# Performance work log

Hardware: AMD Instinct MI355X
Metric: run time of the kernel (lower is better)

The kernel has to match this reference:

```python
import jax, jax.numpy as jnp
import numpy as np

MAX_LENGTH = 10
SOS = 0
B, S, H, V = 256, 10, 1024, 32000


def setup_inputs() -> dict:
    key = jax.random.key(0)
    ks = jax.random.split(key, 16)
    p = lambda k, shp: (jax.random.normal(k, shp, dtype=jnp.float32) * 0.02)
    return {
        "encoder_outputs": jax.random.normal(ks[0], (B, S, H), dtype=jnp.float32),
        "encoder_hidden": jax.random.normal(ks[1], (1, B, H), dtype=jnp.float32),
        "target_tensor": jax.random.randint(ks[2], (B, MAX_LENGTH), 0, V),
        "emb": p(ks[3], (V, H)),
        "Wa": p(ks[4], (H, H)), "ba": p(ks[5], (H,)),
        "Ua": p(ks[6], (H, H)), "bua": p(ks[7], (H,)),
        "Va": p(ks[8], (1, H)), "bva": p(ks[9], (1,)),
        "W_ih": p(ks[10], (3 * H, 2 * H)), "W_hh": p(ks[11], (3 * H, H)),
        "b_ih": p(ks[12], (3 * H,)), "b_hh": p(ks[13], (3 * H,)),
        "W_out": p(ks[14], (V, H)), "b_out": p(ks[15], (V,)),
    }


def reference(encoder_outputs, encoder_hidden, target_tensor, emb, Wa, ba, Ua, bua,
              Va, bva, W_ih, W_hh, b_ih, b_hh, W_out, b_out):
    # Teacher forcing: input tokens are [SOS, tgt_0, ..., tgt_{T-2}]
    tokens = jnp.concatenate(
        [jnp.zeros((B, 1), dtype=target_tensor.dtype) + SOS,
         target_tensor[:, : MAX_LENGTH - 1]], axis=1)  # [B,T]
    keys = encoder_outputs                              # [B,S,H]
    keysW = jnp.einsum('bsh,oh->bso', keys, Wa) + ba    # Wa(keys), hoisted (step-invariant)

    def step(h, tok):                                   # h: [B,H], tok: [B]
        e = emb[tok]                                    # [B,H] (dropout in eval mode = identity)
        q = h @ Ua.T + bua                              # Ua(query): [B,H]
        score = jnp.tanh(keysW + q[:, None, :]) @ Va[0] + bva[0]  # [B,S]
        w = jax.nn.softmax(score, axis=1)               # softmax over seq dim
        ctx = jnp.einsum('bs,bsh->bh', w, keys)         # [B,H]
        x = jnp.concatenate([e, ctx], axis=1)           # [B,2H]
        gi = x @ W_ih.T + b_ih                          # [B,3H]
        gh = h @ W_hh.T + b_hh                          # [B,3H]
        r = jax.nn.sigmoid(gi[:, :H] + gh[:, :H])
        z = jax.nn.sigmoid(gi[:, H:2 * H] + gh[:, H:2 * H])
        n = jnp.tanh(gi[:, 2 * H:] + r * gh[:, 2 * H:])
        h_new = (1.0 - z) * n + z * h
        logits = h_new @ W_out.T + b_out                # [B,V]
        return h_new, (logits, w)

    h0 = encoder_hidden[0]                              # [B,H]
    h_last, (logits, attns) = jax.lax.scan(step, h0, tokens.T)  # logits:[T,B,V], attns:[T,B,S]
    dec_out = jax.nn.log_softmax(jnp.transpose(logits, (1, 0, 2)), axis=-1)  # [B,T,V]
    attentions = jnp.transpose(attns, (1, 0, 2)).reshape(B, MAX_LENGTH * S, 1)  # cat over dim=1
    return dec_out, h_last[None], attentions
```

## Files before the change

kernel.cpp:

```cpp
#include <hip/hip_runtime.h>
#include <hip/hip_bf16.h>
#include <math.h>

#define B_ 256
#define S_ 10
#define H_ 1024
#define V_ 32000
#define T_ 10

typedef __bf16 bf16x8 __attribute__((ext_vector_type(8)));
typedef float f32x4 __attribute__((ext_vector_type(4)));
typedef unsigned short u16;

__device__ inline u16 f2bu(float x) {
    __hip_bfloat16 b = __float2bfloat16(x);
    return *reinterpret_cast<unsigned short*>(&b);
}
__device__ inline float bu2f(u16 x) {
    unsigned u = (unsigned)x << 16;
    return __uint_as_float(u);
}

template<int BM, int BN, int BK, bool SCATTER, bool LSE, bool OUT16>
__global__ __launch_bounds__(256)
void gemm_bt(const u16* __restrict__ A, const u16* __restrict__ B,
             float* __restrict__ C, const float* __restrict__ bias,
             float* __restrict__ lse,
             int M, int N, int K, int ldc, int sb, int st)
{
    constexpr int WM = BM / 2, WN = BN / 2;
    constexpr int AT = WM / 16, BTT = WN / 16;
    constexpr int KS = BK / 32;

    constexpr int STG  = (BM + BN) * BK;
    constexpr int EPI  = 4 * 16 * (WN + 4) * 4;
    constexpr int SMEM = (2 * STG * 2) > EPI ? (2 * STG * 2) : EPI;
    __shared__ __align__(16) char smem[SMEM];
    u16* buf0 = (u16*)smem;
    u16* buf1 = buf0 + STG;

    const int tid  = threadIdx.x;
    const int wave = tid >> 6;
    const int lane = tid & 63;
    const int wm   = (wave >> 1) * WM;
    const int wn   = (wave & 1) * WN;

    int id  = blockIdx.y * gridDim.x + blockIdx.x;
    int nwg = gridDim.x * gridDim.y;
    int swz = id;
    if ((nwg & 7) == 0) swz = (id & 7) * (nwg >> 3) + (id >> 3);
    const int bm = (swz % gridDim.x) * BM;
    const int bn = (swz / gridDim.x) * BN;

    const int l16 = lane & 15;
    const int lk8 = (lane >> 4) * 8;

    f32x4 acc[AT][BTT];
#pragma unroll
    for (int i = 0; i < AT; ++i)
#pragma unroll
        for (int j = 0; j < BTT; ++j) {
            f32x4 z = {0.f, 0.f, 0.f, 0.f};
            acc[i][j] = z;
        }

    constexpr int ROUNDS_A = (BM * BK) / 2048;
    constexpr int ROUNDS_B = (BN * BK) / 2048;

    auto stage = [&](u16* dstA, int k0) {
        u16* dstB = dstA + BM * BK;
#pragma unroll
        for (int r = 0; r < ROUNDS_A; ++r) {
            int e   = r * 2048 + tid * 8;
            int row = e / BK;
            int kk  = e % BK;
            const u16* gp = A + (size_t)(bm + row) * K + k0 + kk;
            u16* lp = dstA + r * 2048 + wave * 512;
            __builtin_amdgcn_global_load_lds(
                (const __attribute__((address_space(1))) void*)gp,
                (__attribute__((address_space(3))) void*)lp, 16, 0, 0);
        }
        if constexpr (ROUNDS_B == 0) {
            if (tid < (BN * BK) / 8) {
                int e   = tid * 8;
                int row = e / BK;
                int kk  = e % BK;
                const u16* gp = B + (size_t)(bn + row) * K + k0 + kk;
                u16* lp = dstB + wave * 512;
                __builtin_amdgcn_global_load_lds(
                    (const __attribute__((address_space(1))) void*)gp,
                    (__attribute__((address_space(3))) void*)lp, 16, 0, 0);
            }
        } else {
#pragma unroll
            for (int r = 0; r < ROUNDS_B; ++r) {
                int e   = r * 2048 + tid * 8;
                int row = e / BK;
                int kk  = e % BK;
                const u16* gp = B + (size_t)(bn + row) * K + k0 + kk;
                u16* lp = dstB + r * 2048 + wave * 512;
                __builtin_amdgcn_global_load_lds(
                    (const __attribute__((address_space(1))) void*)gp,
                    (__attribute__((address_space(3))) void*)lp, 16, 0, 0);
            }
        }
    };

    const int nt = K / BK;
    stage(buf0, 0);
    asm volatile("s_waitcnt vmcnt(0)\n\ts_barrier" ::: "memory");

    int cur = 0;
    for (int t = 0; t < nt; ++t) {
        u16* As = cur ? buf1 : buf0;
        u16* Bs = As + BM * BK;
        u16* nxt = cur ? buf0 : buf1;
        if (t + 1 < nt) stage(nxt, (t + 1) * BK);

        bf16x8 af[KS][AT], bf[KS][BTT];
#pragma unroll
        for (int ks = 0; ks < KS; ++ks) {
#pragma unroll
            for (int i = 0; i < AT; ++i)
                af[ks][i] = *(const bf16x8*)(As + (wm + i * 16 + l16) * BK + ks * 32 + lk8);
#pragma unroll
            for (int j = 0; j < BTT; ++j)
                bf[ks][j] = *(const bf16x8*)(Bs + (wn + j * 16 + l16) * BK + ks * 32 + lk8);
        }
#pragma unroll
        for (int ks = 0; ks < KS; ++ks)
#pragma unroll
            for (int i = 0; i < AT; ++i)
#pragma unroll
                for (int j = 0; j < BTT; ++j)
                    acc[i][j] = __builtin_amdgcn_mfma_f32_16x16x32_bf16(
                        af[ks][i], bf[ks][j], acc[i][j], 0, 0, 0);

        if (t + 1 < nt) {
            asm volatile("s_waitcnt vmcnt(0)\n\ts_barrier" ::: "memory");
            cur ^= 1;
        }
    }
    __syncthreads();

    float (*eps)[16][WN + 4] = reinterpret_cast<float (*)[16][WN + 4]>(smem);
    constexpr int C4  = WN / 4;
    constexpr int RPI = 64 / C4;
    constexpr int STEPS = 16 / RPI;
    const int chunk = lane & (C4 - 1);
    const int rg    = lane / C4;
    const int col   = bn + wn + chunk * 4;
    const int lr4   = (lane >> 4) * 4;

    f32x4 bias4 = {0.f, 0.f, 0.f, 0.f};
    if (bias) bias4 = *(const f32x4*)(bias + col);

#pragma unroll
    for (int i = 0; i < AT; ++i) {
#pragma unroll
        for (int j = 0; j < BTT; ++j)
#pragma unroll
            for (int r = 0; r < 4; ++r)
                eps[wave][lr4 + r][j * 16 + l16] = acc[i][j][r];
#pragma unroll
        for (int s = 0; s < STEPS; ++s) {
            int rowL = s * RPI + rg;
            f32x4 v = *(const f32x4*)&eps[wave][rowL][chunk * 4];
            v += bias4;
            int row = bm + wm + i * 16 + rowL;
            size_t off;
            if constexpr (SCATTER)
                off = (size_t)(row & 255) * sb + (size_t)(row >> 8) * st + col;
            else
                off = (size_t)row * ldc + col;
            if constexpr (OUT16) {
                ushort4 o = {f2bu(v[0]), f2bu(v[1]), f2bu(v[2]), f2bu(v[3])};
                *(ushort4*)((u16*)C + off) = o;
            } else if constexpr (SCATTER) {
                __builtin_nontemporal_store(v, (f32x4*)(C + off));
            } else {
                *(f32x4*)(C + off) = v;
            }
            if constexpr (LSE) {
                float es = expf(v[0]) + expf(v[1]) + expf(v[2]) + expf(v[3]);
#pragma unroll
                for (int o = C4 / 2; o > 0; o >>= 1)
                    es += __shfl_xor(es, o, 64);
                if (chunk == 0) atomicAdd(&lse[row], es);
            }
        }
    }
}

__global__ __launch_bounds__(256)
void attn_gru(const float* __restrict__ keysW, const float* __restrict__ qgh,
              const float* __restrict__ Va, const float* __restrict__ bva,
              const float* __restrict__ gie_t, const u16* __restrict__ KW2,
              float* __restrict__ h, u16* __restrict__ Hall_t,
              float* __restrict__ hlast, float* __restrict__ attn_out, int t)
{
    const int b = blockIdx.x;
    const int tid = threadIdx.x;
    const int lane = tid & 63, wave = tid >> 6;
    const float* qb = qgh + (size_t)b * 4096;
    const float* kW = keysW + (size_t)b * S_ * H_;

    float vh[4], qh[4];
#pragma unroll
    for (int j = 0; j < 4; ++j) {
        int hh = tid + j * 256;
        vh[j] = Va[hh]; qh[j] = qb[hh];
    }

    __shared__ float lred[4][S_];
    __shared__ float wsm[S_];

#pragma unroll
    for (int s = 0; s < S_; ++s) {
        float p = 0.f;
#pragma unroll
        for (int j = 0; j < 4; ++j)
            p += vh[j] * tanhf(kW[s * H_ + tid + j * 256] + qh[j]);
        for (int off = 32; off > 0; off >>= 1) p += __shfl_down(p, off, 64);
        if (lane == 0) lred[wave][s] = p;
    }
    __syncthreads();
    if (tid == 0) {
        float sc[S_], mx = -1e30f;
        for (int s = 0; s < S_; ++s) {
            sc[s] = lred[0][s] + lred[1][s] + lred[2][s] + lred[3][s] + bva[0];
            mx = fmaxf(mx, sc[s]);
        }
        float sum = 0.f;
        for (int s = 0; s < S_; ++s) { sc[s] = expf(sc[s] - mx); sum += sc[s]; }
        float inv = 1.f / sum;
        for (int s = 0; s < S_; ++s) wsm[s] = sc[s] * inv;
    }
    __syncthreads();
    if (tid < S_) attn_out[(size_t)b * 100 + t * 10 + tid] = wsm[tid];

    const int i4 = tid * 4;
    float ar[4] = {0,0,0,0}, az[4] = {0,0,0,0}, an[4] = {0,0,0,0};
    const u16* kwb = KW2 + (size_t)b * (S_ * 3072);
#pragma unroll
    for (int s = 0; s < S_; ++s) {
        float w = wsm[s];
        const u16* kws = kwb + s * 3072;
        ushort4 vr = *(const ushort4*)(kws + i4);
        ushort4 vz = *(const ushort4*)(kws + 1024 + i4);
        ushort4 vn = *(const ushort4*)(kws + 2048 + i4);
        ar[0] += w * bu2f(vr.x); ar[1] += w * bu2f(vr.y);
        ar[2] += w * bu2f(vr.z); ar[3] += w * bu2f(vr.w);
        az[0] += w * bu2f(vz.x); az[1] += w * bu2f(vz.y);
        az[2] += w * bu2f(vz.z); az[3] += w * bu2f(vz.w);
        an[0] += w * bu2f(vn.x); an[1] += w * bu2f(vn.y);
        an[2] += w * bu2f(vn.z); an[3] += w * bu2f(vn.w);
    }

    const float* ghp = qgh + (size_t)b * 4096 + 1024;
    const float* gip = gie_t + (size_t)b * 3072;
    float4 g_r = *(const float4*)(gip + i4);
    float4 g_z = *(const float4*)(gip + 1024 + i4);
    float4 g_n = *(const float4*)(gip + 2048 + i4);
    float4 h_r = *(const float4*)(ghp + i4);
    float4 h_z = *(const float4*)(ghp + 1024 + i4);
    float4 h_n = *(const float4*)(ghp + 2048 + i4);
    float4 hold = *(const float4*)(h + (size_t)b * 1024 + i4);

    float hv[4];
#pragma unroll
    for (int r = 0; r < 4; ++r) {
        float gr = (&g_r.x)[r] + ar[r];
        float gz = (&g_z.x)[r] + az[r];
        float gn = (&g_n.x)[r] + an[r];
        float rr = 1.f / (1.f + expf(-(gr + (&h_r.x)[r])));
        float zz = 1.f / (1.f + expf(-(gz + (&h_z.x)[r])));
        float nn = tanhf(gn + rr * (&h_n.x)[r]);
        hv[r] = (1.f - zz) * nn + zz * (&hold.x)[r];
    }
    float4 hv4 = {hv[0], hv[1], hv[2], hv[3]};
    *(float4*)(h + (size_t)b * 1024 + i4) = hv4;
    ushort4 hb = {f2bu(hv[0]), f2bu(hv[1]), f2bu(hv[2]), f2bu(hv[3])};
    *(ushort4*)(Hall_t + (size_t)b * 1024 + i4) = hb;
    if (hlast) *(float4*)(hlast + (size_t)b * 1024 + i4) = hv4;
}

__global__ __launch_bounds__(256)
void lse_finish(float* __restrict__ dec, const float* __restrict__ lse)
{
    const int r = blockIdx.x;
    const int b = r & 255, t = r >> 8;
    const float l = logf(lse[r]);
    float* row = dec + (size_t)b * (T_ * V_) + (size_t)t * V_;
    for (int i = threadIdx.x * 4; i < V_; i += 1024) {
        f32x4 v = __builtin_nontemporal_load((const f32x4*)(row + i));
        v -= l;
        __builtin_nontemporal_store(v, (f32x4*)(row + i));
    }
}

__global__ __launch_bounds__(256)
void cvt_f32_bf16(const float* __restrict__ src, u16* __restrict__ dst, int n)
{
    int i = (blockIdx.x * 256 + threadIdx.x) * 4;
    float4 v = *(const float4*)(src + i);
    ushort4 o;
    o.x = f2bu(v.x); o.y = f2bu(v.y); o.z = f2bu(v.z); o.w = f2bu(v.w);
    *(ushort4*)(dst + i) = o;
}

__global__ __launch_bounds__(256)
void split_wih(const float* __restrict__ Wih, u16* __restrict__ We, u16* __restrict__ W2)
{
    int i = (blockIdx.x * 256 + threadIdx.x) * 4;
    int row = i >> 11, col = i & 2047;
    float4 v = *(const float4*)(Wih + i);
    ushort4 o;
    o.x = f2bu(v.x); o.y = f2bu(v.y); o.z = f2bu(v.z); o.w = f2bu(v.w);
    u16* dst = (col < 1024) ? (We + (size_t)row * 1024 + col)
                            : (W2 + (size_t)row * 1024 + (col - 1024));
    *(ushort4*)dst = o;
}

__global__ __launch_bounds__(256)
void build_bias1(const float* __restrict__ bua, const float* __restrict__ bhh,
                 float* __restrict__ bias1, float* __restrict__ lse)
{
    int i = blockIdx.x * 256 + threadIdx.x;
    bias1[i] = (i < 1024) ? bua[i] : bhh[i - 1024];
    if (i < 2560) lse[i] = 0.f;
}

__global__ __launch_bounds__(256)
void init_h(const float* __restrict__ eh, float* __restrict__ h, u16* __restrict__ hbf)
{
    int i = blockIdx.x * 256 + threadIdx.x;
    float v = eh[i];
    h[i] = v;
    hbf[i] = f2bu(v);
}

__global__ __launch_bounds__(256)
void gather_emb(const float* __restrict__ emb, const int* __restrict__ tgt,
                u16* __restrict__ E)
{
    int idx = blockIdx.x * 256 + threadIdx.x;
    int i4 = idx * 4;
    int m = i4 >> 10, col = i4 & 1023;
    int t = m >> 8, b = m & 255;
    int tok = (t == 0) ? 0 : tgt[b * 10 + t - 1];
    float4 v = *(const float4*)(emb + (size_t)tok * 1024 + col);
    ushort4 o;
    o.x = f2bu(v.x); o.y = f2bu(v.y); o.z = f2bu(v.z); o.w = f2bu(v.w);
    *(ushort4*)(E + (size_t)m * 1024 + col) = o;
}

extern "C" void kernel_launch(void* const* d_in, const int* in_sizes, int n_in,
                              void* d_out, int out_size, void* d_ws, size_t ws_size,
                              hipStream_t stream)
{
    const float* enc_out = (const float*)d_in[0];
    const float* enc_hid = (const float*)d_in[1];
    const int*   tgt     = (const int*)d_in[2];
    const float* emb     = (const float*)d_in[3];
    const float* Wa      = (const float*)d_in[4];
    const float* ba      = (const float*)d_in[5];
    const float* Ua      = (const float*)d_in[6];
    const float* bua     = (const float*)d_in[7];
    const float* Va      = (const float*)d_in[8];
    const float* bva     = (const float*)d_in[9];
    const float* Wih     = (const float*)d_in[10];
    const float* Whh     = (const float*)d_in[11];
    const float* bih     = (const float*)d_in[12];
    const float* bhh     = (const float*)d_in[13];
    const float* Wout    = (const float*)d_in[14];
    const float* bout    = (const float*)d_in[15];

    float* dec   = (float*)d_out;
    float* hlast = dec + (size_t)B_ * T_ * V_;
    float* attn  = hlast + (size_t)B_ * H_;

    char* ws = (char*)d_ws;
    size_t used = 0;
    auto alloc = [&](size_t bytes) {
        char* p = ws + used;
        used += (bytes + 255) & ~(size_t)255;
        return p;
    };
    u16*  Wout_b = (u16*)alloc((size_t)V_ * H_ * 2);
    u16*  Wa_b   = (u16*)alloc((size_t)H_ * H_ * 2);
    u16*  W1_b   = (u16*)alloc((size_t)4096 * H_ * 2);
    u16*  We_b   = (u16*)alloc((size_t)3072 * H_ * 2);
    u16*  W2_b   = (u16*)alloc((size_t)3072 * H_ * 2);
    u16*  keys_b = (u16*)alloc((size_t)2560 * H_ * 2);
    u16*  E_b    = (u16*)alloc((size_t)2560 * H_ * 2);
    u16*  Hall_b = (u16*)alloc((size_t)2560 * H_ * 2);
    u16*  h_b    = (u16*)alloc((size_t)B_ * H_ * 2);
    u16*  KW2    = (u16*)alloc((size_t)2560 * 3072 * 2);
    float* keysW = (float*)alloc((size_t)2560 * H_ * 4);
    float* gie   = (float*)alloc((size_t)2560 * 3072 * 4);
    float* qgh   = (float*)alloc((size_t)B_ * 4096 * 4);
    float* hbuf  = (float*)alloc((size_t)B_ * H_ * 4);
    float* bias1 = (float*)alloc(4096 * 4);
    float* lse   = (float*)alloc(2560 * 4);
    if (used > ws_size) return;

    cvt_f32_bf16<<<V_ * H_ / 1024, 256, 0, stream>>>(Wout, Wout_b, V_ * H_);
    cvt_f32_bf16<<<H_ * H_ / 1024, 256, 0, stream>>>(Wa, Wa_b, H_ * H_);
    cvt_f32_bf16<<<H_ * H_ / 1024, 256, 0, stream>>>(Ua, W1_b, H_ * H_);
    cvt_f32_bf16<<<3072 * H_ / 1024, 256, 0, stream>>>(Whh, W1_b + (size_t)1024 * H_, 3072 * H_);
    split_wih<<<3072 * 2048 / 1024, 256, 0, stream>>>(Wih, We_b, W2_b);
    cvt_f32_bf16<<<2560 * H_ / 1024, 256, 0, stream>>>(enc_out, keys_b, 2560 * H_);
    gather_emb<<<2560, 256, 0, stream>>>(emb, tgt, E_b);
    build_bias1<<<16, 256, 0, stream>>>(bua, bhh, bias1, lse);
    init_h<<<1024, 256, 0, stream>>>(enc_hid, hbuf, h_b);

    {
        dim3 g(2560 / 128, 1024 / 128);
        gemm_bt<128, 128, 32, false, false, false><<<g, 256, 0, stream>>>(
            keys_b, Wa_b, keysW, ba, nullptr, 2560, 1024, 1024, 1024, 0, 0);
    }
    {
        dim3 g(2560 / 128, 3072 / 128);
        gemm_bt<128, 128, 32, false, false, false><<<g, 256, 0, stream>>>(
            E_b, We_b, gie, bih, nullptr, 2560, 3072, 1024, 3072, 0, 0);
    }
    {
        dim3 g(2560 / 128, 3072 / 128);
        gemm_bt<128, 128, 32, false, false, true><<<g, 256, 0, stream>>>(
            keys_b, W2_b, (float*)KW2, nullptr, nullptr, 2560, 3072, 1024, 3072, 0, 0);
    }

    for (int t = 0; t < T_; ++t) {
        const u16* hsrc = (t == 0) ? h_b : (Hall_b + (size_t)(t - 1) * B_ * H_);
        {
            dim3 g(256 / 64, 4096 / 32);
            gemm_bt<64, 32, 32, false, false, false><<<g, 256, 0, stream>>>(
                hsrc, W1_b, qgh, bias1, nullptr, 256, 4096, 1024, 4096, 0, 0);
        }
        attn_gru<<<256, 256, 0, stream>>>(
            keysW, qgh, Va, bva, gie + (size_t)t * 256 * 3072, KW2, hbuf,
            Hall_b + (size_t)t * B_ * H_, (t == T_ - 1) ? hlast : nullptr,
            attn, t);
    }

    {
        dim3 g(2560 / 128, 32000 / 128);
        gemm_bt<128, 128, 32, true, true, false><<<g, 256, 0, stream>>>(
            Hall_b, Wout_b, dec, bout, lse, 2560, 32000, 1024,
            0, T_ * V_ , V_ );
    }
    lse_finish<<<2560, 256, 0, stream>>>(dec, lse);
}
```

Before: 1.276 ms.

## Triple-buffer GEMM staging with partial vmcnt waits for deeper prefetch

Replaces the double-buffered LDS pipeline in the bf16 GEMM with three rotating stage buffers, prefetching two K-tiles ahead. Each iteration waits only until the current tile's loads have landed (using counted vmcnt waits that depend on how many newer tiles are in flight), instead of draining all outstanding loads. The intent is to hide more global-load latency behind MFMA work. In exchange it uses 1.5x the LDS, which may lower occupancy, and it adds an extra barrier per iteration.

```diff
diff --git a/kernel.cpp b/kernel.cpp
--- a/kernel.cpp
+++ b/kernel.cpp
@@ -21,6 +21,18 @@
     return __uint_as_float(u);
 }
 
+template<int N>
+__device__ __forceinline__ void wait_vmcnt() {
+    static_assert(N==0||N==1||N==2||N==3||N==4||N==6||N==8, "unsupported vmcnt");
+    if constexpr (N == 8)      asm volatile("s_waitcnt vmcnt(8)" ::: "memory");
+    else if constexpr (N == 6) asm volatile("s_waitcnt vmcnt(6)" ::: "memory");
+    else if constexpr (N == 4) asm volatile("s_waitcnt vmcnt(4)" ::: "memory");
+    else if constexpr (N == 3) asm volatile("s_waitcnt vmcnt(3)" ::: "memory");
+    else if constexpr (N == 2) asm volatile("s_waitcnt vmcnt(2)" ::: "memory");
+    else if constexpr (N == 1) asm volatile("s_waitcnt vmcnt(1)" ::: "memory");
+    else                       asm volatile("s_waitcnt vmcnt(0)" ::: "memory");
+}
+
 template<int BM, int BN, int BK, bool SCATTER, bool LSE, bool OUT16>
 __global__ __launch_bounds__(256)
 void gemm_bt(const u16* __restrict__ A, const u16* __restrict__ B,
@@ -34,10 +46,8 @@
 
     constexpr int STG  = (BM + BN) * BK;
     constexpr int EPI  = 4 * 16 * (WN + 4) * 4;
-    constexpr int SMEM = (2 * STG * 2) > EPI ? (2 * STG * 2) : EPI;
+    constexpr int SMEM = (3 * STG * 2) > EPI ? (3 * STG * 2) : EPI;
     __shared__ __align__(16) char smem[SMEM];
-    u16* buf0 = (u16*)smem;
-    u16* buf1 = buf0 + STG;
 
     const int tid  = threadIdx.x;
     const int wave = tid >> 6;
@@ -66,6 +76,10 @@
 
     constexpr int ROUNDS_A = (BM * BK) / 2048;
     constexpr int ROUNDS_B = (BN * BK) / 2048;
+
+    constexpr int BW   = (ROUNDS_B == 0) ? (BN * BK) / 512 : 4;
+    constexpr int LPSb = ROUNDS_A + (ROUNDS_B ? ROUNDS_B : 1);
+    constexpr int LPSn = ROUNDS_A + ROUNDS_B;
 
     auto stage = [&](u16* dstA, int k0) {
         u16* dstB = dstA + BM * BK;
@@ -106,17 +120,39 @@
         }
     };
 
+    auto wait_tile = [&](int newer) {
+        if constexpr (LPSb == LPSn) {
+            if (newer == 2)      wait_vmcnt<2 * LPSn>();
+            else if (newer == 1) wait_vmcnt<LPSn>();
+            else                 wait_vmcnt<0>();
+        } else {
+            if (wave < BW) {
+                if (newer == 2)      wait_vmcnt<2 * LPSb>();
+                else if (newer == 1) wait_vmcnt<LPSb>();
+                else                 wait_vmcnt<0>();
+            } else {
+                if (newer == 2)      wait_vmcnt<2 * LPSn>();
+                else if (newer == 1) wait_vmcnt<LPSn>();
+                else                 wait_vmcnt<0>();
+            }
+        }
+    };
+
     const int nt = K / BK;
-    stage(buf0, 0);
-    asm volatile("s_waitcnt vmcnt(0)\n\ts_barrier" ::: "memory");
-
-    int cur = 0;
+    u16* b0 = (u16*)smem;
+    u16* b1 = b0 + STG;
+    u16* b2 = b1 + STG;
+    stage(b0, 0);
+    stage(b1, BK);
+
     for (int t = 0; t < nt; ++t) {
-        u16* As = cur ? buf1 : buf0;
-        u16* Bs = As + BM * BK;
-        u16* nxt = cur ? buf0 : buf1;
-        if (t + 1 < nt) stage(nxt, (t + 1) * BK);
-
+        if (t + 2 < nt) stage(b2, (t + 2) * BK);
+        int newer = nt - 1 - t; if (newer > 2) newer = 2;
+        wait_tile(newer);
+        asm volatile("s_barrier" ::: "memory");
+
+        u16* As = b0;
+        u16* Bs = b0 + BM * BK;
         bf16x8 af[KS][AT], bf[KS][BTT];
 #pragma unroll
         for (int ks = 0; ks < KS; ++ks) {
@@ -136,10 +172,8 @@
                     acc[i][j] = __builtin_amdgcn_mfma_f32_16x16x32_bf16(
                         af[ks][i], bf[ks][j], acc[i][j], 0, 0, 0);
 
-        if (t + 1 < nt) {
-            asm volatile("s_waitcnt vmcnt(0)\n\ts_barrier" ::: "memory");
-            cur ^= 1;
-        }
+        asm volatile("s_barrier" ::: "memory");
+        u16* tmp = b0; b0 = b1; b1 = b2; b2 = tmp;
     }
     __syncthreads();
 
```

After: 1.261 ms. About the same (-1.2%).
